# Performance work log

Hardware: AMD Instinct MI355X
Metric: run time of the kernel (lower is better)

The kernel has to match this reference:

```python
import jax, jax.numpy as jnp
import numpy as np

B, N_LINES, C_FEAT = 16, 200, 64
H_IMG = W_IMG = 256
NUM_BINS = 32
LINE_LENGTH = 64
LINE_LENGTH_MINUS_1_HALF = (LINE_LENGTH - 1) / 2.0
MIN_CONTINUOUS_DISTANCE = 6.0
FUNCTION_AMPLITUDE = 0.43
FUNCTION_SLOPE = 0.5
EPS = 1e-05


def _unnorm(coord, size):
    # torch grid_sample align_corners=False: pixel = ((g + 1) * size - 1) / 2
    return ((coord + 1.0) * size - 1.0) * 0.5


def _gather2d(img, yi, xi, valid):
    # img (B,C,H,W); yi/xi (B,N,L) int32 in-range; zeros padding via valid mask
    g = jax.vmap(lambda im, yy, xx: im[:, yy, xx])(img, yi, xi)  # (B,C,N,L)
    return g * valid[:, None].astype(img.dtype)


def grid_sample_nearest(img, grid):
    _, _, H, W = img.shape
    x = _unnorm(grid[..., 0], W)
    y = _unnorm(grid[..., 1], H)
    xi = jnp.round(x).astype(jnp.int32)
    yi = jnp.round(y).astype(jnp.int32)
    valid = (xi >= 0) & (xi < W) & (yi >= 0) & (yi < H)
    return _gather2d(img, jnp.clip(yi, 0, H - 1), jnp.clip(xi, 0, W - 1), valid)


def grid_sample_bilinear(img, grid):
    _, _, H, W = img.shape
    x = _unnorm(grid[..., 0], W)
    y = _unnorm(grid[..., 1], H)
    x0 = jnp.floor(x)
    y0 = jnp.floor(y)
    wx1 = x - x0
    wy1 = y - y0
    x0i = x0.astype(jnp.int32)
    y0i = y0.astype(jnp.int32)
    out = jnp.zeros(img.shape[:2] + grid.shape[1:3], dtype=img.dtype)
    for dx, wx in ((0, 1.0 - wx1), (1, wx1)):
        for dy, wy in ((0, 1.0 - wy1), (1, wy1)):
            xi = x0i + dx
            yi = y0i + dy
            valid = (xi >= 0) & (xi < W) & (yi >= 0) & (yi < H)
            g = _gather2d(img, jnp.clip(yi, 0, H - 1), jnp.clip(xi, 0, W - 1), valid)
            out = out + g * (wx * wy)[:, None]
    return out


def setup_inputs() -> dict:
    key = jax.random.key(0)
    k = jax.random.split(key, 6)
    image = jax.random.uniform(k[0], (B, 3, H_IMG, W_IMG), dtype=jnp.float32)
    feature = jax.random.normal(k[1], (B, C_FEAT, H_IMG, W_IMG), dtype=jnp.float32)
    pose = jnp.concatenate([
        jnp.tile(jnp.eye(3, dtype=jnp.float32).reshape(1, 9), (B, 1)),
        jnp.tile(jnp.array([[0.0, 0.0, 0.5]], dtype=jnp.float32), (B, 1)),
    ], axis=-1)  # identity rotation, 0.5m in front of camera
    camera_data = jnp.tile(
        jnp.array([[float(W_IMG), float(H_IMG), 300.0, 300.0, 128.0, 128.0]], dtype=jnp.float32),
        (B, 1))  # [w, h, fx, fy, cx, cy]
    centers = jax.random.normal(k[2], (B, N_LINES, 3), dtype=jnp.float32) * 0.05
    normals = jax.random.normal(k[3], (B, N_LINES, 3), dtype=jnp.float32)
    normals = normals / jnp.linalg.norm(normals, axis=-1, keepdims=True)
    dists = jnp.full((B, N_LINES, 2), 0.02, dtype=jnp.float32)
    template_view = jnp.concatenate([centers, normals, dists], axis=-1)  # (B,N,8)
    fore_hist = jax.random.uniform(k[4], (B, NUM_BINS ** 3), dtype=jnp.float32)
    back_hist = jax.random.uniform(k[5], (B, NUM_BINS ** 3), dtype=jnp.float32)
    return {"image": image, "feature": feature,
            "init_body2view_pose_data": pose, "camera_data": camera_data,
            "template_view": template_view, "fore_hist": fore_hist,
            "back_hist": back_hist}


def reference(image, feature, init_body2view_pose_data, camera_data, template_view,
              fore_hist, back_hist):
    R = init_body2view_pose_data[:, :9].reshape(-1, 3, 3)
    t = init_body2view_pose_data[:, 9:]
    centers_in_body = template_view[..., :3]
    normals_in_body = template_view[..., 3:6]
    fg_dist = template_view[..., 6]
    bg_dist = template_view[..., 7]

    # transform / rotate (p3d @ R^T + t)
    centers_in_view = jnp.einsum('bnj,bij->bni', centers_in_body, R) + t[:, None]
    normals_in_view = jnp.einsum('bnj,bij->bni', normals_in_body, R)

    # project_p3d
    z = centers_in_view[..., 2]
    valid1 = z > 1e-4
    p2d = centers_in_view[..., :2] / jnp.maximum(z, 1e-4)[..., None]
    f = camera_data[:, 2:4]
    c = camera_data[:, 4:6]
    size = camera_data[:, :2]
    centers_in_image = p2d * f[:, None] + c[:, None]
    in_b = (centers_in_image >= 0) & (centers_in_image <= size[:, None] - 1)
    centers_valid = valid1 & in_b[..., 0] & in_b[..., 1]

    n2 = normals_in_view[..., :2]
    normals_in_image = n2 / jnp.maximum(jnp.linalg.norm(n2, axis=-1, keepdims=True), 1e-12)

    cur_fg = fg_dist * f[:, 0:1] / z
    cur_bg = bg_dist * f[:, 0:1] / z
    continuous_distance = jnp.minimum(cur_fg, cur_bg)  # fscale = 1 in forward
    valid_data_line = (continuous_distance >= MIN_CONTINUOUS_DISTANCE) & centers_valid

    width, height = feature.shape[2], feature.shape[3]

    # build search-line sample points: (B,N,L,2)
    step = jnp.arange(LINE_LENGTH, dtype=centers_in_image.dtype) - LINE_LENGTH_MINUS_1_HALF
    points = centers_in_image[:, :, None, :] + step[None, None, :, None] * normals_in_image[:, :, None, :]

    def _in_bounds(p):
        return (p[..., 0] >= 0) & (p[..., 0] < width) & (p[..., 1] >= 0) & (p[..., 1] < height)

    valid_data_line = valid_data_line & _in_bounds(points[:, :, 0]) & _in_bounds(points[:, :, -1])

    grid = jnp.stack([points[..., 0] / width * 2 - 1,
                      points[..., 1] / height * 2 - 1], axis=-1)

    # nearest sample of RGB image -> histogram fg/bg probability lookup
    lines_image = grid_sample_nearest(image, grid)  # (B,3,N,L)
    bins = jnp.clip((lines_image * NUM_BINS).astype(jnp.int32), 0, NUM_BINS - 1)
    hist_idx = (bins[:, 0] * NUM_BINS + bins[:, 1]) * NUM_BINS + bins[:, 2]  # (B,N,L)
    pf = jax.vmap(lambda h, i: h[i])(fore_hist, hist_idx)
    pb = jax.vmap(lambda h, i: h[i])(back_hist, hist_idx)
    zero_idx = (pf < EPS) & (pb < EPS)
    pf = jnp.where(zero_idx, EPS, pf)
    pb = jnp.where(zero_idx, EPS, pb)
    psum = pf + pb
    pf = pf / psum  # lines_image_pf_segments (second eps/normalize pass is a no-op)
    pb = pb / psum  # lines_image_pb_segments

    lines_feature = grid_sample_bilinear(feature, grid)  # (B,C,N,L)
    lines_amplitude = jnp.full(pf.shape[:2], FUNCTION_AMPLITUDE, dtype=feature.dtype)
    lines_slope = jnp.full(pf.shape[:2], FUNCTION_SLOPE, dtype=feature.dtype)

    return (normals_in_image, centers_in_image, centers_in_body, pf, pb,
            valid_data_line, lines_amplitude, lines_slope, lines_feature)
```

## Files before the change

kernel.cpp:

```cpp
#include <hip/hip_runtime.h>

#define BN     16
#define NLINES 200
#define CFEAT  64
#define HIMG   256
#define WIMG   256
#define LLEN   64
#define NBINS  32

#define O_NORM   0
#define O_CIMG   6400
#define O_CBODY  12800
#define O_PF     22400
#define O_PB     227200
#define O_VALID  432000
#define O_AMP    435200
#define O_SLOPE  438400
#define O_FEAT   441600

#define NPTS (BN*NLINES*LLEN)

struct LineGeom {
  float cix, ciy;
  float nix, niy;
  float cb0, cb1, cb2;
  bool  vdl;
};

__device__ __forceinline__ LineGeom compute_line(
    const float* __restrict__ pose, const float* __restrict__ cam,
    const float* __restrict__ tv, int b, int n)
{
  const float* P = pose + b*12;
  float R00=P[0],R01=P[1],R02=P[2];
  float R10=P[3],R11=P[4],R12=P[5];
  float R20=P[6],R21=P[7],R22=P[8];
  float t0=P[9], t1=P[10], t2=P[11];
  const float* C = cam + b*6;
  float sx=C[0], sy=C[1], fx=C[2], fy=C[3];
  float cx=C[4], cy=C[5];
  const float* T = tv + (b*NLINES + n)*8;
  float cb0=T[0], cb1=T[1], cb2=T[2];
  float nb0=T[3], nb1=T[4], nb2=T[5];
  float fg=T[6],  bg=T[7];

  float cv0 = R00*cb0 + R01*cb1 + R02*cb2 + t0;
  float cv1 = R10*cb0 + R11*cb1 + R12*cb2 + t1;
  float cv2 = R20*cb0 + R21*cb1 + R22*cb2 + t2;
  float nv0 = R00*nb0 + R01*nb1 + R02*nb2;
  float nv1 = R10*nb0 + R11*nb1 + R12*nb2;

  float z  = cv2;
  float zc = fmaxf(z, 1e-4f);
  float cix = (cv0/zc)*fx + cx;
  float ciy = (cv1/zc)*fy + cy;
  bool inb = (cix >= 0.f) && (cix <= sx - 1.f) && (ciy >= 0.f) && (ciy <= sy - 1.f);
  bool centers_valid = (z > 1e-4f) && inb;

  float nrm = fmaxf(sqrtf(nv0*nv0 + nv1*nv1), 1e-12f);
  float nix = nv0/nrm, niy = nv1/nrm;

  float contd = fminf(fg*fx/z, bg*fx/z);
  bool vdl = (contd >= 6.0f) && centers_valid;

  float px0 = cix + (-31.5f)*nix, py0 = ciy + (-31.5f)*niy;
  float px1 = cix + ( 31.5f)*nix, py1 = ciy + ( 31.5f)*niy;
  vdl = vdl && (px0 >= 0.f) && (px0 < 256.f) && (py0 >= 0.f) && (py0 < 256.f)
            && (px1 >= 0.f) && (px1 < 256.f) && (py1 >= 0.f) && (py1 < 256.f);

  LineGeom g;
  g.cix = cix; g.ciy = ciy; g.nix = nix; g.niy = niy;
  g.cb0 = cb0; g.cb1 = cb1; g.cb2 = cb2; g.vdl = vdl;
  return g;
}

__device__ __forceinline__ void point_xy(const LineGeom& g, int i, float& x, float& y)
{
  float s  = (float)i - 31.5f;
  float px = g.cix + s*g.nix;
  float py = g.ciy + s*g.niy;
  float gx = px/256.0f*2.0f - 1.0f;
  float gy = py/256.0f*2.0f - 1.0f;
  x = ((gx + 1.0f)*256.0f - 1.0f)*0.5f;
  y = ((gy + 1.0f)*256.0f - 1.0f)*0.5f;
}

__global__ __launch_bounds__(256)
void contour_points_kernel(const float* __restrict__ image,
                           const float* __restrict__ pose,
                           const float* __restrict__ cam,
                           const float* __restrict__ tv,
                           const float* __restrict__ fore,
                           const float* __restrict__ back,
                           float* __restrict__ out)
{
  int tid = blockIdx.x*256 + threadIdx.x;
  int i  = tid & 63;
  int ln = tid >> 6;
  int n  = ln % NLINES;
  int b  = ln / NLINES;

  LineGeom g = compute_line(pose, cam, tv, b, n);

  float x, y;
  point_xy(g, i, x, y);

  float xr = rintf(x), yr = rintf(y);
  int xi = (int)xr, yi = (int)yr;
  bool v = (xi >= 0) && (xi < WIMG) && (yi >= 0) && (yi < HIMG);
  int xc = min(max(xi, 0), WIMG-1), yc = min(max(yi, 0), HIMG-1);
  const float* ib = image + (size_t)b*3*HIMG*WIMG + yc*WIMG + xc;
  float r0 = v ? ib[0]           : 0.f;
  float r1 = v ? ib[HIMG*WIMG]   : 0.f;
  float r2 = v ? ib[2*HIMG*WIMG] : 0.f;

  int b0 = min(max((int)(r0*32.f), 0), NBINS-1);
  int b1 = min(max((int)(r1*32.f), 0), NBINS-1);
  int b2 = min(max((int)(r2*32.f), 0), NBINS-1);
  int hidx = (b0*NBINS + b1)*NBINS + b2;

  float pf = fore[b*NBINS*NBINS*NBINS + hidx];
  float pb = back[b*NBINS*NBINS*NBINS + hidx];
  if (pf < 1e-5f && pb < 1e-5f) { pf = 1e-5f; pb = 1e-5f; }
  float ps = pf + pb;
  pf /= ps; pb /= ps;

  out[O_PF + ln*LLEN + i] = pf;
  out[O_PB + ln*LLEN + i] = pb;

  if (i == 0) {
    out[O_NORM  + ln*2 + 0] = g.nix;
    out[O_NORM  + ln*2 + 1] = g.niy;
    out[O_CIMG  + ln*2 + 0] = g.cix;
    out[O_CIMG  + ln*2 + 1] = g.ciy;
    out[O_CBODY + ln*3 + 0] = g.cb0;
    out[O_CBODY + ln*3 + 1] = g.cb1;
    out[O_CBODY + ln*3 + 2] = g.cb2;
    out[O_VALID + ln] = g.vdl ? 1.0f : 0.0f;
    out[O_AMP   + ln] = 0.43f;
    out[O_SLOPE + ln] = 0.5f;
  }
}

__global__ __launch_bounds__(256)
void contour_gather4_kernel(const float* __restrict__ feature,
                            const float* __restrict__ pose,
                            const float* __restrict__ cam,
                            const float* __restrict__ tv,
                            float* __restrict__ out)
{
  int bid = blockIdx.x;
  int xcd = bid & 7;
  int q   = bid >> 3;
  int j   = q % 50;
  int ug  = q / 50;
  int u   = ug*8 + xcd;
  int b   = u >> 4;
  int c   = (u & 15) << 2;

  int idx = j*256 + (int)threadIdx.x;
  int n   = idx >> 6;
  int i   = idx & 63;

  LineGeom g = compute_line(pose, cam, tv, b, n);
  float x, y;
  point_xy(g, i, x, y);

  float x0f = floorf(x), y0f = floorf(y);
  float wx1 = x - x0f, wy1 = y - y0f;
  float wx0 = 1.0f - wx1, wy0 = 1.0f - wy1;
  int x0 = (int)x0f, y0 = (int)y0f;
  int x1 = x0 + 1,  y1 = y0 + 1;
  bool vx0 = (x0 >= 0) && (x0 < WIMG);
  bool vx1 = (x1 >= 0) && (x1 < WIMG);
  bool vy0 = (y0 >= 0) && (y0 < HIMG);
  bool vy1 = (y1 >= 0) && (y1 < HIMG);

  int xc0 = min(max(x0, 0), WIMG-1);
  int xc1 = min(max(x1, 0), WIMG-1);
  int xb  = min(max(x0, 0), WIMG-2);
  int yb0 = min(max(y0, 0), HIMG-1);
  int yb1 = min(max(y1, 0), HIMG-1);

  float fx0 = vx0 ? wx0 : 0.f;
  float fx1 = vx1 ? wx1 : 0.f;
  float wa = ((xc0 == xb)   ? fx0 : 0.f) + ((xc1 == xb)   ? fx1 : 0.f);
  float wb = ((xc0 == xb+1) ? fx0 : 0.f) + ((xc1 == xb+1) ? fx1 : 0.f);
  float wyA = vy0 ? wy0 : 0.f;
  float wyB = vy1 ? wy1 : 0.f;

  const float* base = feature + ((size_t)(b*CFEAT + c) << 16);
  int o0 = yb0*WIMG + xb;
  int o1 = yb1*WIMG + xb;

  float2 r0[4], r1[4];
  #pragma unroll
  for (int k = 0; k < 4; ++k) {
    __builtin_memcpy(&r0[k], base + (size_t)k*65536 + o0, 8);
    __builtin_memcpy(&r1[k], base + (size_t)k*65536 + o1, 8);
  }

  size_t ob = (size_t)O_FEAT + (((size_t)(b*CFEAT + c))*NLINES + n)*LLEN + i;
  #pragma unroll
  for (int k = 0; k < 4; ++k) {
    float v = wyA*(wa*r0[k].x + wb*r0[k].y)
            + wyB*(wa*r1[k].x + wb*r1[k].y);
    out[ob + (size_t)k*(NLINES*LLEN)] = v;
  }
}

extern "C" void kernel_launch(void* const* d_in, const int* in_sizes, int n_in,
                              void* d_out, int out_size, void* d_ws, size_t ws_size,
                              hipStream_t stream) {
  const float* image   = (const float*)d_in[0];
  const float* feature = (const float*)d_in[1];
  const float* pose    = (const float*)d_in[2];
  const float* cam     = (const float*)d_in[3];
  const float* tv      = (const float*)d_in[4];
  const float* fore    = (const float*)d_in[5];
  const float* back    = (const float*)d_in[6];
  float* out = (float*)d_out;

  contour_points_kernel<<<NPTS/256, 256, 0, stream>>>(
      image, pose, cam, tv, fore, back, out);
  contour_gather4_kernel<<<(BN*CFEAT*NLINES*LLEN)/(4*256), 256, 0, stream>>>(
      feature, pose, cam, tv, out);
}
```

Before: 414.4 us.

## Fuse histogram and feature-gather kernels, gather eight channels per thread

```diff
diff --git a/kernel.cpp b/kernel.cpp
--- a/kernel.cpp
+++ b/kernel.cpp
@@ -86,68 +86,14 @@
 }
 
 __global__ __launch_bounds__(256)
-void contour_points_kernel(const float* __restrict__ image,
-                           const float* __restrict__ pose,
-                           const float* __restrict__ cam,
-                           const float* __restrict__ tv,
-                           const float* __restrict__ fore,
-                           const float* __restrict__ back,
-                           float* __restrict__ out)
-{
-  int tid = blockIdx.x*256 + threadIdx.x;
-  int i  = tid & 63;
-  int ln = tid >> 6;
-  int n  = ln % NLINES;
-  int b  = ln / NLINES;
-
-  LineGeom g = compute_line(pose, cam, tv, b, n);
-
-  float x, y;
-  point_xy(g, i, x, y);
-
-  float xr = rintf(x), yr = rintf(y);
-  int xi = (int)xr, yi = (int)yr;
-  bool v = (xi >= 0) && (xi < WIMG) && (yi >= 0) && (yi < HIMG);
-  int xc = min(max(xi, 0), WIMG-1), yc = min(max(yi, 0), HIMG-1);
-  const float* ib = image + (size_t)b*3*HIMG*WIMG + yc*WIMG + xc;
-  float r0 = v ? ib[0]           : 0.f;
-  float r1 = v ? ib[HIMG*WIMG]   : 0.f;
-  float r2 = v ? ib[2*HIMG*WIMG] : 0.f;
-
-  int b0 = min(max((int)(r0*32.f), 0), NBINS-1);
-  int b1 = min(max((int)(r1*32.f), 0), NBINS-1);
-  int b2 = min(max((int)(r2*32.f), 0), NBINS-1);
-  int hidx = (b0*NBINS + b1)*NBINS + b2;
-
-  float pf = fore[b*NBINS*NBINS*NBINS + hidx];
-  float pb = back[b*NBINS*NBINS*NBINS + hidx];
-  if (pf < 1e-5f && pb < 1e-5f) { pf = 1e-5f; pb = 1e-5f; }
-  float ps = pf + pb;
-  pf /= ps; pb /= ps;
-
-  out[O_PF + ln*LLEN + i] = pf;
-  out[O_PB + ln*LLEN + i] = pb;
-
-  if (i == 0) {
-    out[O_NORM  + ln*2 + 0] = g.nix;
-    out[O_NORM  + ln*2 + 1] = g.niy;
-    out[O_CIMG  + ln*2 + 0] = g.cix;
-    out[O_CIMG  + ln*2 + 1] = g.ciy;
-    out[O_CBODY + ln*3 + 0] = g.cb0;
-    out[O_CBODY + ln*3 + 1] = g.cb1;
-    out[O_CBODY + ln*3 + 2] = g.cb2;
-    out[O_VALID + ln] = g.vdl ? 1.0f : 0.0f;
-    out[O_AMP   + ln] = 0.43f;
-    out[O_SLOPE + ln] = 0.5f;
-  }
-}
-
-__global__ __launch_bounds__(256)
-void contour_gather4_kernel(const float* __restrict__ feature,
-                            const float* __restrict__ pose,
-                            const float* __restrict__ cam,
-                            const float* __restrict__ tv,
-                            float* __restrict__ out)
+void contour_fused_kernel(const float* __restrict__ feature,
+                          const float* __restrict__ image,
+                          const float* __restrict__ pose,
+                          const float* __restrict__ cam,
+                          const float* __restrict__ tv,
+                          const float* __restrict__ fore,
+                          const float* __restrict__ back,
+                          float* __restrict__ out)
 {
   int bid = blockIdx.x;
   int xcd = bid & 7;
@@ -155,8 +101,9 @@
   int j   = q % 50;
   int ug  = q / 50;
   int u   = ug*8 + xcd;
-  int b   = u >> 4;
-  int c   = (u & 15) << 2;
+  int b   = u >> 3;
+  int c8  = u & 7;
+  int c   = c8 << 3;
 
   int idx = j*256 + (int)threadIdx.x;
   int n   = idx >> 6;
@@ -188,23 +135,67 @@
   float wb = ((xc0 == xb+1) ? fx0 : 0.f) + ((xc1 == xb+1) ? fx1 : 0.f);
   float wyA = vy0 ? wy0 : 0.f;
   float wyB = vy1 ? wy1 : 0.f;
+  float w00 = wyA*wa, w01 = wyA*wb;
+  float w10 = wyB*wa, w11 = wyB*wb;
 
   const float* base = feature + ((size_t)(b*CFEAT + c) << 16);
   int o0 = yb0*WIMG + xb;
   int o1 = yb1*WIMG + xb;
 
-  float2 r0[4], r1[4];
+  float2 r0[8], r1[8];
   #pragma unroll
-  for (int k = 0; k < 4; ++k) {
+  for (int k = 0; k < 8; ++k) {
     __builtin_memcpy(&r0[k], base + (size_t)k*65536 + o0, 8);
     __builtin_memcpy(&r1[k], base + (size_t)k*65536 + o1, 8);
   }
 
+  if (c8 == (b & 7)) {
+    int ln = b*NLINES + n;
+
+    float xr = rintf(x), yr = rintf(y);
+    int xi = (int)xr, yi = (int)yr;
+    bool v = (xi >= 0) && (xi < WIMG) && (yi >= 0) && (yi < HIMG);
+    int xc = min(max(xi, 0), WIMG-1), yc = min(max(yi, 0), HIMG-1);
+    const float* ib = image + (size_t)b*3*HIMG*WIMG + yc*WIMG + xc;
+    float r0i = v ? ib[0]           : 0.f;
+    float r1i = v ? ib[HIMG*WIMG]   : 0.f;
+    float r2i = v ? ib[2*HIMG*WIMG] : 0.f;
+
+    int b0 = min(max((int)(r0i*32.f), 0), NBINS-1);
+    int b1 = min(max((int)(r1i*32.f), 0), NBINS-1);
+    int b2 = min(max((int)(r2i*32.f), 0), NBINS-1);
+    int hidx = (b0*NBINS + b1)*NBINS + b2;
+
+    float pf = fore[b*NBINS*NBINS*NBINS + hidx];
+    float pb = back[b*NBINS*NBINS*NBINS + hidx];
+    if (pf < 1e-5f && pb < 1e-5f) { pf = 1e-5f; pb = 1e-5f; }
+    float ps = pf + pb;
+    pf /= ps; pb /= ps;
+
+    out[O_PF + ln*LLEN + i] = pf;
+    out[O_PB + ln*LLEN + i] = pb;
+
+    if (i == 0) {
+      out[O_NORM  + ln*2 + 0] = g.nix;
+      out[O_NORM  + ln*2 + 1] = g.niy;
+      out[O_CIMG  + ln*2 + 0] = g.cix;
+      out[O_CIMG  + ln*2 + 1] = g.ciy;
+      out[O_CBODY + ln*3 + 0] = g.cb0;
+      out[O_CBODY + ln*3 + 1] = g.cb1;
+      out[O_CBODY + ln*3 + 2] = g.cb2;
+      out[O_VALID + ln] = g.vdl ? 1.0f : 0.0f;
+      out[O_AMP   + ln] = 0.43f;
+      out[O_SLOPE + ln] = 0.5f;
+    }
+  }
+
   size_t ob = (size_t)O_FEAT + (((size_t)(b*CFEAT + c))*NLINES + n)*LLEN + i;
   #pragma unroll
-  for (int k = 0; k < 4; ++k) {
-    float v = wyA*(wa*r0[k].x + wb*r0[k].y)
-            + wyB*(wa*r1[k].x + wb*r1[k].y);
+  for (int k = 0; k < 8; ++k) {
+    float v = fmaf(w00, r0[k].x,
+              fmaf(w01, r0[k].y,
+              fmaf(w10, r1[k].x,
+                   w11 * r1[k].y)));
     out[ob + (size_t)k*(NLINES*LLEN)] = v;
   }
 }
@@ -221,8 +212,6 @@
   const float* back    = (const float*)d_in[6];
   float* out = (float*)d_out;
 
-  contour_points_kernel<<<NPTS/256, 256, 0, stream>>>(
-      image, pose, cam, tv, fore, back, out);
-  contour_gather4_kernel<<<(BN*CFEAT*NLINES*LLEN)/(4*256), 256, 0, stream>>>(
-      feature, pose, cam, tv, out);
-}
+  contour_fused_kernel<<<(BN*CFEAT*NLINES*LLEN)/(8*256), 256, 0, stream>>>(
+      feature, image, pose, cam, tv, fore, back, out);
+}
```

Result: faster. 405.1 us (-2.3%).
